# Performance work log

Measured on AMD Instinct MI355X. Metric: run time of the kernel, lower is better.

Reference implementation:

```python
import jax, jax.numpy as jnp
import numpy as np

SOFTCAP = 50.0
EPS = 1e-6
N_HEADS, D_HEAD = 16, 64


def _rms(x, w):
    return x * jax.lax.rsqrt(jnp.mean(x * x, axis=-1, keepdims=True) + EPS) * w


def _rope(x, cos, sin):
    # Faithful to source: apply_rope uses x.size(1) as the position axis, but is
    # called on (B, H, T, Dh) tensors, so positions are indexed by HEAD index.
    n = x.shape[1]
    x1, x2 = x[..., 0::2], x[..., 1::2]
    c = cos[:n][None, :, None, :]
    s = sin[:n][None, :, None, :]
    return jnp.stack([x1 * c - x2 * s, x1 * s + x2 * c], axis=-1).reshape(x.shape)


def setup_inputs() -> dict:
    key = jax.random.key(0)
    ks = jax.random.split(key, 12)
    L, D, H, Dh, Dff, V, B, T = 6, 1024, N_HEADS, D_HEAD, 4096, 32000, 1, 1024
    r = lambda k, shape: jax.random.normal(k, shape, dtype=jnp.float32) * 0.02
    return {
        'x': jax.random.randint(ks[0], (B, T), 0, V, dtype=jnp.int32),
        'embed': r(ks[1], (V, D)),
        'ln1': jnp.ones((L, D), jnp.float32),
        'Wq': r(ks[2], (L, H * Dh, D)),
        'Wk': r(ks[3], (L, H * Dh, D)),
        'Wv': r(ks[4], (L, H * Dh, D)),
        'Wo': r(ks[5], (L, D, H * Dh)),
        'qn': jnp.ones((L, Dh), jnp.float32),
        'kn': jnp.ones((L, Dh), jnp.float32),
        'ln2': jnp.ones((L, D), jnp.float32),
        'Wg': r(ks[6], (L, Dff, D)),
        'Wu': r(ks[7], (L, Dff, D)),
        'Wd': r(ks[8], (L, D, Dff)),
        'ln_out': jnp.ones((D,), jnp.float32),
    }


def reference(x, embed, ln1, Wq, Wk, Wv, Wo, qn, kn, ln2, Wg, Wu, Wd, ln_out):
    B, T = x.shape
    H, Dh = N_HEADS, D_HEAD
    scale = Dh ** -0.5
    # RoPE tables (theta=10000)
    freqs = 1.0 / (10000.0 ** (jnp.arange(0, Dh, 2, dtype=jnp.float32) / Dh))
    ang = jnp.arange(T, dtype=jnp.float32)[:, None] * freqs[None, :]
    cos, sin = jnp.cos(ang), jnp.sin(ang)
    mask = jnp.triu(jnp.ones((T, T), dtype=bool), k=1)  # True above diagonal

    h = embed[x]  # (B, T, D)

    def block(h, p):
        l1, wq, wk, wv, wo, qnw, knw, l2, wg, wu, wd = p
        hn = _rms(h, l1)
        q = (hn @ wq.T).reshape(B, T, H, Dh).transpose(0, 2, 1, 3)  # (B,H,T,Dh)
        k = (hn @ wk.T).reshape(B, T, H, Dh).transpose(0, 2, 1, 3)
        v = (hn @ wv.T).reshape(B, T, H, Dh).transpose(0, 2, 1, 3)
        q = _rope(_rms(q, qnw), cos, sin)
        k = _rope(_rms(k, knw), cos, sin)
        scores = jnp.einsum('bhtd,bhsd->bhts', q, k) * scale
        scores = SOFTCAP * jnp.tanh(scores / SOFTCAP)
        scores = jnp.where(mask[None, None], -jnp.inf, scores)
        attn = jax.nn.softmax(scores, axis=-1)
        o = jnp.einsum('bhts,bhsd->bhtd', attn, v)
        o = o.transpose(0, 2, 1, 3).reshape(B, T, H * Dh)
        h = h + o @ wo.T
        hn2 = _rms(h, l2)
        h = h + (jax.nn.silu(hn2 @ wg.T) * (hn2 @ wu.T)) @ wd.T
        return h, None

    h, _ = jax.lax.scan(block, h, (ln1, Wq, Wk, Wv, Wo, qn, kn, ln2, Wg, Wu, Wd))
    # tied embed/head
    logits = _rms(h, ln_out) @ embed.T  # (B, T, V)
    return logits
```

## Files before the change

kernel.cpp:

```cpp
#include <hip/hip_runtime.h>
#include <math.h>
#include <type_traits>

typedef __bf16 bf16_t;
typedef bf16_t bf16x4 __attribute__((ext_vector_type(4)));
typedef bf16_t bf16x8 __attribute__((ext_vector_type(8)));
typedef float  f32x4  __attribute__((ext_vector_type(4)));

#define RMS_EPS 1e-6f

enum { EP_STORE = 0, EP_RESID = 1, EP_SPLIT = 2, EP_SILU = 3 };

template<int V> using IC = std::integral_constant<int, V>;

static __device__ __forceinline__ f32x4 mfma16(bf16x8 a, bf16x8 b, f32x4 c) {
    return __builtin_amdgcn_mfma_f32_16x16x32_bf16(a, b, c, 0, 0, 0);
}

#define GLDS(gp, lp) __builtin_amdgcn_global_load_lds( \
    (const __attribute__((address_space(1))) void*)(gp), \
    (__attribute__((address_space(3))) void*)(lp), 16, 0, 0)

template<int N> static __device__ __forceinline__ void vmwait() {
    if constexpr (N == 0)      asm volatile("s_waitcnt vmcnt(0)" ::: "memory");
    else if constexpr (N == 2) asm volatile("s_waitcnt vmcnt(2)" ::: "memory");
    else if constexpr (N == 3) asm volatile("s_waitcnt vmcnt(3)" ::: "memory");
    else if constexpr (N == 4) asm volatile("s_waitcnt vmcnt(4)" ::: "memory");
    else if constexpr (N == 6) asm volatile("s_waitcnt vmcnt(6)" ::: "memory");
    else if constexpr (N == 8) asm volatile("s_waitcnt vmcnt(8)" ::: "memory");
    __builtin_amdgcn_sched_barrier(0);
}
static __device__ __forceinline__ void bar() { __builtin_amdgcn_s_barrier(); }

template<int BM, int BN, int PLANES, int EPIL>
__global__ __launch_bounds__(256, (PLANES >= 2 && BM == 128) ? 3 : 4)
void gemm_bf16(const bf16_t* __restrict__ Ah, const bf16_t* __restrict__ Al,
               const bf16_t* __restrict__ Bh,
               float* __restrict__ Cf, bf16_t* __restrict__ Ch, bf16_t* __restrict__ Cl,
               int K, int lda, int ldb, int ldc, long long sC)
{
    constexpr int ASZ = BM * 32, BSZ = BN * 32;
    constexpr int NLD = (BM / 64) * (PLANES >= 2 ? 2 : 1) + (BN / 64);
    __shared__ __align__(16) bf16_t sAh[2][ASZ], sBh[2][BSZ];
    __shared__ __align__(16) bf16_t sAl[PLANES >= 2 ? 2 : 1][PLANES >= 2 ? ASZ : 8];

    const int gx = gridDim.x;
    int id = blockIdx.x + gx * blockIdx.y;
    if (gridDim.z == 1) {
        int nwg = gx * gridDim.y;
        int q = nwg >> 3, r = nwg & 7;
        int xcd = id & 7, ix = id >> 3;
        id = (xcd < r ? xcd * (q + 1) : r * (q + 1) + (xcd - r) * q) + ix;
    }
    const int bm = id % gx, bn = id / gx;
    const int row0 = bm * BM, col0 = bn * BN;

    const size_t kofs = (size_t)blockIdx.z * K;
    Ah += kofs;  Bh += kofs;
    if constexpr (PLANES >= 2) Al += kofs;

    const int tid = threadIdx.x, lane = tid & 63, wave = tid >> 6;
    const int lr = lane & 15, lg = lane >> 4;
    constexpr int WM = BM / 2, WN = BN / 2, MF = WM / 16, NF = WN / 16;
    const int wm = wave >> 1, wn = wave & 1;

    f32x4 acc[MF][NF];
    #pragma unroll
    for (int m = 0; m < MF; ++m)
        #pragma unroll
        for (int n = 0; n < NF; ++n) acc[m][n] = (f32x4){0.f, 0.f, 0.f, 0.f};

    auto stage = [&](int k0, auto pc) {
        constexpr int p = decltype(pc)::value;
        #pragma unroll
        for (int i = wave; i < BM / 16; i += 4) {
            int s = i * 64 + lane, rr = s >> 2, c = s & 3;
            size_t go = (size_t)(row0 + rr) * lda + k0 + ((c ^ ((rr >> 1) & 3)) << 3);
            GLDS(Ah + go, &sAh[p][i * 512]);
            if constexpr (PLANES >= 2) GLDS(Al + go, &sAl[p][i * 512]);
        }
        #pragma unroll
        for (int i = wave; i < BN / 16; i += 4) {
            int s = i * 64 + lane, rr = s >> 2, c = s & 3;
            size_t go = (size_t)(col0 + rr) * ldb + k0 + ((c ^ ((rr >> 1) & 3)) << 3);
            GLDS(Bh + go, &sBh[p][i * 512]);
        }
    };

    auto compute = [&](auto pc) {
        constexpr int p = decltype(pc)::value;
        bf16x8 ahf[MF], alf[MF], bhf[NF];
        #pragma unroll
        for (int m = 0; m < MF; ++m) {
            int rr = wm * WM + m * 16 + lr;
            int by = rr * 64 + ((lg ^ ((rr >> 1) & 3)) << 4);
            ahf[m] = *(const bf16x8*)((const char*)&sAh[p][0] + by);
            if constexpr (PLANES >= 2)
                alf[m] = *(const bf16x8*)((const char*)&sAl[p][0] + by);
        }
        #pragma unroll
        for (int n = 0; n < NF; ++n) {
            int rr = wn * WN + n * 16 + lr;
            int by = rr * 64 + ((lg ^ ((rr >> 1) & 3)) << 4);
            bhf[n] = *(const bf16x8*)((const char*)&sBh[p][0] + by);
        }
        #pragma unroll
        for (int m = 0; m < MF; ++m)
            #pragma unroll
            for (int n = 0; n < NF; ++n) {
                acc[m][n] = mfma16(ahf[m], bhf[n], acc[m][n]);
                if constexpr (PLANES >= 2)
                    acc[m][n] = mfma16(alf[m], bhf[n], acc[m][n]);
            }
    };

    stage(0, IC<0>{});
    int k0 = 32;
    for (; k0 + 32 < K; k0 += 64) {
        stage(k0, IC<1>{});
        vmwait<NLD>(); bar();
        compute(IC<0>{});
        bar();
        stage(k0 + 32, IC<0>{});
        vmwait<NLD>(); bar();
        compute(IC<1>{});
        bar();
    }
    stage(k0, IC<1>{});
    vmwait<NLD>(); bar();
    compute(IC<0>{});
    bar();
    vmwait<0>(); bar();
    compute(IC<1>{});

    #pragma unroll
    for (int m = 0; m < MF; ++m)
        #pragma unroll
        for (int n = 0; n < NF; ++n)
            #pragma unroll
            for (int r = 0; r < 4; ++r) {
                int grow = row0 + wm * WM + m * 16 + lg * 4 + r;
                int gcol = col0 + wn * WN + n * 16 + lr;
                float v = acc[m][n][r];
                if constexpr (EPIL == EP_SILU) {
                    float pv = __shfl_xor(v, 1, 64);
                    if (!(lr & 1)) {
                        float s = (v / (1.0f + expf(-v))) * pv;
                        size_t off = (size_t)grow * ldc + (gcol >> 1);
                        Ch[off] = (bf16_t)s;
                    }
                } else {
                    size_t off = (size_t)blockIdx.z * sC + (size_t)grow * ldc + gcol;
                    if constexpr (EPIL == EP_STORE) {
                        Cf[off] = v;
                    } else if constexpr (EPIL == EP_RESID) {
                        Cf[off] += v;
                    } else {
                        bf16_t hb = (bf16_t)v;
                        Ch[off] = hb;
                        Cl[off] = (bf16_t)(v - (float)hb);
                    }
                }
            }
}

__global__ __launch_bounds__(256, 3)
void gemm_logits(const bf16_t* __restrict__ Ah, const bf16_t* __restrict__ Bh,
                 float* __restrict__ Cf)
{
    constexpr int lda = 1024, ldb = 1024, ldc = 32000;
    __shared__ __align__(16) bf16_t sA[3][128 * 32], sB[3][128 * 32];

    const int gx = gridDim.x;
    int id = blockIdx.x + gx * blockIdx.y;
    {
        int nwg = gx * gridDim.y;
        int q = nwg >> 3, r = nwg & 7;
        int xcd = id & 7, ix = id >> 3;
        id = (xcd < r ? xcd * (q + 1) : r * (q + 1) + (xcd - r) * q) + ix;
    }
    const int bm = id % gx, bn = id / gx;
    const int row0 = bm * 128, col0 = bn * 128;

    const int tid = threadIdx.x, lane = tid & 63, wave = tid >> 6;
    const int lr = lane & 15, lg = lane >> 4;
    const int wm = wave >> 1, wn = wave & 1;

    f32x4 acc[4][4];
    #pragma unroll
    for (int m = 0; m < 4; ++m)
        #pragma unroll
        for (int n = 0; n < 4; ++n) acc[m][n] = (f32x4){0.f, 0.f, 0.f, 0.f};

    auto stage = [&](int k0, int p) {
        #pragma unroll
        for (int i = wave; i < 8; i += 4) {
            int s = i * 64 + lane, rr = s >> 2, c = s & 3;
            size_t go = (size_t)(row0 + rr) * lda + k0 + ((c ^ ((rr >> 1) & 3)) << 3);
            GLDS(Ah + go, &sA[p][i * 512]);
        }
        #pragma unroll
        for (int i = wave; i < 8; i += 4) {
            int s = i * 64 + lane, rr = s >> 2, c = s & 3;
            size_t go = (size_t)(col0 + rr) * ldb + k0 + ((c ^ ((rr >> 1) & 3)) << 3);
            GLDS(Bh + go, &sB[p][i * 512]);
        }
    };

    auto compute = [&](int p) {
        bf16x8 af[4], bf[4];
        #pragma unroll
        for (int m = 0; m < 4; ++m) {
            int rr = wm * 64 + m * 16 + lr;
            int by = rr * 64 + ((lg ^ ((rr >> 1) & 3)) << 4);
            af[m] = *(const bf16x8*)((const char*)&sA[p][0] + by);
        }
        #pragma unroll
        for (int n = 0; n < 4; ++n) {
            int rr = wn * 64 + n * 16 + lr;
            int by = rr * 64 + ((lg ^ ((rr >> 1) & 3)) << 4);
            bf[n] = *(const bf16x8*)((const char*)&sB[p][0] + by);
        }
        #pragma unroll
        for (int m = 0; m < 4; ++m)
            #pragma unroll
            for (int n = 0; n < 4; ++n)
                acc[m][n] = mfma16(af[m], bf[n], acc[m][n]);
    };

    stage(0, 0);
    stage(32, 1);
    for (int j = 0; j < 30; ++j) {
        stage(32 * (j + 2), (j + 2) % 3);
        vmwait<8>(); bar();
        compute(j % 3);
        bar();
    }
    vmwait<4>(); bar();
    compute(0);
    vmwait<0>(); bar();
    compute(1);

    #pragma unroll
    for (int m = 0; m < 4; ++m)
        #pragma unroll
        for (int n = 0; n < 4; ++n)
            #pragma unroll
            for (int r = 0; r < 4; ++r) {
                int grow = row0 + wm * 64 + m * 16 + lg * 4 + r;
                int gcol = col0 + wn * 64 + n * 16 + lr;
                Cf[(size_t)grow * ldc + gcol] = acc[m][n][r];
            }
}

__global__ __launch_bounds__(256)
void reduce4_rms(const float* __restrict__ p, float* __restrict__ h,
                 const float* __restrict__ w, bf16_t* __restrict__ outh)
{
    int row = blockIdx.x, tid = threadIdx.x;
    size_t i = (size_t)row * 256 + tid;
    const size_t S = (1024 * 1024) / 4;
    f32x4 a = ((const f32x4*)p)[i];
    f32x4 b = ((const f32x4*)p)[i + S];
    f32x4 c = ((const f32x4*)p)[i + 2 * S];
    f32x4 d = ((const f32x4*)p)[i + 3 * S];
    f32x4 hv = ((const f32x4*)h)[i];
    #pragma unroll
    for (int j = 0; j < 4; ++j) hv[j] += (a[j] + b[j]) + (c[j] + d[j]);
    ((f32x4*)h)[i] = hv;

    float ss = hv[0]*hv[0] + hv[1]*hv[1] + hv[2]*hv[2] + hv[3]*hv[3];
    #pragma unroll
    for (int m = 1; m < 64; m <<= 1) ss += __shfl_xor(ss, m, 64);
    __shared__ float red[4];
    if ((tid & 63) == 0) red[tid >> 6] = ss;
    __syncthreads();
    float tot = red[0] + red[1] + red[2] + red[3];
    float inv = rsqrtf(tot * (1.0f / 1024.0f) + RMS_EPS);
    f32x4 wv = *(const f32x4*)(w + tid * 4);
    bf16x4 hv4;
    #pragma unroll
    for (int j = 0; j < 4; ++j) hv4[j] = (bf16_t)(hv[j] * inv * wv[j]);
    ((bf16x4*)outh)[i] = hv4;
}

__global__ __launch_bounds__(128, 2)
void flash_attn(const bf16_t* __restrict__ qkvh,
                const bf16_t* __restrict__ vTh, const bf16_t* __restrict__ vTl,
                bf16_t* __restrict__ oh)
{
    __shared__ __align__(16) bf16_t sQ[32*64], sK[64*64], sVh[64*64], sVl[64*64];
    __shared__ __align__(16) bf16_t sPh[32*64], sPl[32*64];

    const int px = blockIdx.x;
    const int hh = blockIdx.y;
    const int tid = threadIdx.x, lane = tid & 63, w = tid >> 6;
    const int lr = lane & 15, lg = lane >> 4;

    for (int cc = 0; cc < 2; ++cc) {
        const int qb = cc ? 31 - px : px;
        const int q0 = qb * 32;

        #pragma unroll
        for (int ii = 0; ii < 2; ++ii) {
            int r0 = w * 16 + ii * 8;
            int r  = r0 + (lane >> 3);
            int i  = lane & 7;
            GLDS(qkvh + (size_t)(q0 + r) * 3072 + hh * 64 + ((i ^ (r & 7)) << 3),
                 sQ + r0 * 64);
        }
        __syncthreads();

        bf16x8 qa[2];
        #pragma unroll
        for (int ks = 0; ks < 2; ++ks) {
            int r = w * 16 + lr;
            qa[ks] = *(const bf16x8*)((const char*)sQ + r * 128 +
                                      ((((ks << 2) | lg) ^ (r & 7)) << 4));
        }

        f32x4 o_acc[4];
        #pragma unroll
        for (int n = 0; n < 4; ++n) o_acc[n] = (f32x4){0.f, 0.f, 0.f, 0.f};
        float m_run[4] = {-1e30f, -1e30f, -1e30f, -1e30f};
        float l_run[4] = {0.f, 0.f, 0.f, 0.f};

        const int ntiles = ((q0 + 31) >> 6) + 1;
        for (int t = 0; t < ntiles; ++t) {
            const int kv0 = t * 64;
            #pragma unroll
            for (int ii = 0; ii < 4; ++ii) {
                int r0 = w * 32 + ii * 8;
                int r  = r0 + (lane >> 3);
                int i  = lane & 7;
                GLDS(qkvh + (size_t)(kv0 + r) * 3072 + 1024 + hh * 64 + ((i ^ (r & 7)) << 3),
                     sK + r0 * 64);
                GLDS(vTh + (size_t)(hh * 64 + r) * 1024 + kv0 + ((i ^ (r & 7)) << 3),
                     sVh + r0 * 64);
                GLDS(vTl + (size_t)(hh * 64 + r) * 1024 + kv0 + ((i ^ (r & 7)) << 3),
                     sVl + r0 * 64);
            }
            __syncthreads();

            f32x4 s_acc[4];
            #pragma unroll
            for (int n = 0; n < 4; ++n) s_acc[n] = (f32x4){0.f, 0.f, 0.f, 0.f};
            #pragma unroll
            for (int ks = 0; ks < 2; ++ks)
                #pragma unroll
                for (int n = 0; n < 4; ++n) {
                    int r = n * 16 + lr;
                    bf16x8 kb = *(const bf16x8*)((const char*)sK + r * 128 +
                                                 ((((ks << 2) | lg) ^ (r & 7)) << 4));
                    s_acc[n] = mfma16(qa[ks], kb, s_acc[n]);
                }

            #pragma unroll
            for (int j = 0; j < 4; ++j) {
                int qr = q0 + w * 16 + lg * 4 + j;
                float p[4];
                float mx = -1e30f;
                #pragma unroll
                for (int n = 0; n < 4; ++n) {
                    float v = s_acc[n][j] * 0.125f;
                    v = 50.f * tanhf(v * 0.02f);
                    int key = kv0 + n * 16 + lr;
                    if (key > qr) v = -1e30f;
                    p[n] = v;
                    mx = fmaxf(mx, v);
                }
                #pragma unroll
                for (int m = 1; m < 16; m <<= 1) mx = fmaxf(mx, __shfl_xor(mx, m, 64));
                float mn = fmaxf(m_run[j], mx);
                float ef = __expf(m_run[j] - mn);
                m_run[j] = mn;
                float rs = 0.f;
                #pragma unroll
                for (int n = 0; n < 4; ++n) {
                    float e = expf(p[n] - mn);
                    p[n] = e;
                    rs += e;
                }
                #pragma unroll
                for (int m = 1; m < 16; m <<= 1) rs += __shfl_xor(rs, m, 64);
                l_run[j] = l_run[j] * ef + rs;
                #pragma unroll
                for (int n = 0; n < 4; ++n) o_acc[n][j] *= ef;
                int r = w * 16 + lg * 4 + j;
                #pragma unroll
                for (int n = 0; n < 4; ++n) {
                    int c = n * 16 + lr;
                    int byo = r * 128 + ((((c >> 3) ^ (r & 7)) << 4)) + ((c & 7) << 1);
                    bf16_t hb = (bf16_t)p[n];
                    *(bf16_t*)((char*)sPh + byo) = hb;
                    *(bf16_t*)((char*)sPl + byo) = (bf16_t)(p[n] - (float)hb);
                }
            }

            #pragma unroll
            for (int ks = 0; ks < 2; ++ks) {
                int pr = w * 16 + lr;
                int pby = pr * 128 + ((((ks << 2) | lg) ^ (pr & 7)) << 4);
                bf16x8 pa  = *(const bf16x8*)((const char*)sPh + pby);
                bf16x8 pl_ = *(const bf16x8*)((const char*)sPl + pby);
                #pragma unroll
                for (int n = 0; n < 4; ++n) {
                    int vr = n * 16 + lr;
                    int vby = vr * 128 + ((((ks << 2) | lg) ^ (vr & 7)) << 4);
                    bf16x8 vhf = *(const bf16x8*)((const char*)sVh + vby);
                    bf16x8 vlf = *(const bf16x8*)((const char*)sVl + vby);
                    o_acc[n] = mfma16(pa,  vhf, o_acc[n]);
                    o_acc[n] = mfma16(pl_, vhf, o_acc[n]);
                    o_acc[n] = mfma16(pa,  vlf, o_acc[n]);
                }
            }
            __syncthreads();
        }

        #pragma unroll
        for (int j = 0; j < 4; ++j) {
            float inv = 1.0f / l_run[j];
            int qr = q0 + w * 16 + lg * 4 + j;
            #pragma unroll
            for (int n = 0; n < 4; ++n) {
                size_t off = (size_t)qr * 1024 + hh * 64 + n * 16 + lr;
                oh[off] = (bf16_t)(o_acc[n][j] * inv);
            }
        }
    }
}

__global__ __launch_bounds__(256)
void split_kernel(const float* __restrict__ src, bf16_t* __restrict__ hi,
                  bf16_t* __restrict__ lo)
{
    size_t i = (size_t)blockIdx.x * 256 + threadIdx.x;
    f32x4 v = ((const f32x4*)src)[i];
    bf16x4 hv, lv;
    #pragma unroll
    for (int j = 0; j < 4; ++j) {
        bf16_t hb = (bf16_t)v[j];
        hv[j] = hb;
        lv[j] = (bf16_t)(v[j] - (float)hb);
    }
    ((bf16x4*)hi)[i] = hv;
    if (lo) ((bf16x4*)lo)[i] = lv;
}

__global__ __launch_bounds__(256)
void wsplit_kernel(const float* __restrict__ wq, const float* __restrict__ wk,
                   const float* __restrict__ wv, const float* __restrict__ wo,
                   const float* __restrict__ wg, const float* __restrict__ wu,
                   const float* __restrict__ wd,
                   bf16_t* __restrict__ wAh, bf16_t* __restrict__ wGUh,
                   bf16_t* __restrict__ wdh)
{
    #pragma unroll
    for (int k = 0; k < 4; ++k) {
        int b = blockIdx.x * 4 + k;
        const float* src;
        bf16_t* dst;
        size_t so, doff;
        if (b < 4096) {
            src = b < 1024 ? wq : b < 2048 ? wk : b < 3072 ? wv : wo;
            so = (size_t)(b & 1023) * 256 + threadIdx.x;
            doff = (size_t)b * 256 + threadIdx.x;
            dst = wAh;
        } else if (b < 12288) {
            int bb = b - 4096;
            int row = bb < 4096 ? 2 * bb : 2 * (bb - 4096) + 1;
            src = bb < 4096 ? wg : wu;
            so = (size_t)(bb & 4095) * 256 + threadIdx.x;
            doff = (size_t)row * 256 + threadIdx.x;
            dst = wGUh;
        } else {
            src = wd;
            so = (size_t)(b - 12288) * 256 + threadIdx.x;
            doff = so;
            dst = wdh;
        }
        f32x4 v = ((const f32x4*)src)[so];
        bf16x4 hv;
        #pragma unroll
        for (int j = 0; j < 4; ++j) hv[j] = (bf16_t)v[j];
        ((bf16x4*)dst)[doff] = hv;
    }
}

__global__ __launch_bounds__(256)
void gather_rms(const int* __restrict__ ids, const float* __restrict__ embed,
                const float* __restrict__ w, float* __restrict__ h,
                bf16_t* __restrict__ outh)
{
    int t = blockIdx.x, tid = threadIdx.x;
    int row = ids[t];
    f32x4 v = ((const f32x4*)(embed + (size_t)row * 1024))[tid];
    ((f32x4*)(h + (size_t)t * 1024))[tid] = v;

    float ss = v[0]*v[0] + v[1]*v[1] + v[2]*v[2] + v[3]*v[3];
    #pragma unroll
    for (int m = 1; m < 64; m <<= 1) ss += __shfl_xor(ss, m, 64);
    __shared__ float red[4];
    if ((tid & 63) == 0) red[tid >> 6] = ss;
    __syncthreads();
    float tot = red[0] + red[1] + red[2] + red[3];
    float inv = rsqrtf(tot * (1.0f / 1024.0f) + RMS_EPS);
    f32x4 wv = *(const f32x4*)(w + tid * 4);
    bf16x4 hv;
    #pragma unroll
    for (int j = 0; j < 4; ++j) hv[j] = (bf16_t)(v[j] * inv * wv[j]);
    ((bf16x4*)outh)[(size_t)t * 256 + tid] = hv;
}

__global__ __launch_bounds__(256)
void rmsnorm_split(const float* __restrict__ in, const float* __restrict__ w,
                   bf16_t* __restrict__ outh)
{
    int row = blockIdx.x, tid = threadIdx.x;
    f32x4 v = *(const f32x4*)(in + (size_t)row * 1024 + tid * 4);
    float ss = v[0]*v[0] + v[1]*v[1] + v[2]*v[2] + v[3]*v[3];
    #pragma unroll
    for (int m = 1; m < 64; m <<= 1) ss += __shfl_xor(ss, m, 64);
    __shared__ float red[4];
    if ((tid & 63) == 0) red[tid >> 6] = ss;
    __syncthreads();
    float tot = red[0] + red[1] + red[2] + red[3];
    float inv = rsqrtf(tot * (1.0f / 1024.0f) + RMS_EPS);
    f32x4 wv = *(const f32x4*)(w + tid * 4);
    bf16x4 hv;
    #pragma unroll
    for (int j = 0; j < 4; ++j) hv[j] = (bf16_t)(v[j] * inv * wv[j]);
    ((bf16x4*)outh)[(size_t)row * 256 + tid] = hv;
}

__global__ __launch_bounds__(256)
void rope_transpose(bf16_t* __restrict__ qkvh, bf16_t* __restrict__ qkvl,
                    const float* __restrict__ qn, const float* __restrict__ kn,
                    bf16_t* __restrict__ vTh, bf16_t* __restrict__ vTl)
{
    __shared__ bf16_t tile[32][33];
    int b = blockIdx.x;
    if (b >= 1024) {
        int t2 = b - 1024;
        int z = t2 >> 10, rem = t2 & 1023;
        const bf16_t* in = z ? qkvl : qkvh;
        bf16_t* out      = z ? vTl : vTh;
        int bx = (rem & 31) * 32, by = (rem >> 5) * 32;
        int r = threadIdx.x >> 5, c = threadIdx.x & 31;
        #pragma unroll
        for (int rr = r; rr < 32; rr += 8)
            tile[rr][c] = in[(size_t)(by + rr) * 3072 + 2048 + bx + c];
        __syncthreads();
        #pragma unroll
        for (int rr = r; rr < 32; rr += 8)
            out[(size_t)(bx + rr) * 1024 + by + c] = tile[c][rr];
        return;
    }

    int t = b, tid = threadIdx.x;
    int hh = tid >> 4;
    int i  = (tid & 15) * 4;
    size_t qb = ((size_t)t * 3072 + hh * 64 + i) >> 2;
    size_t kb = qb + (1024 >> 2);

    int p0 = i >> 1;
    float f0 = powf(10000.f, -(float)p0 / 32.f);
    float f1 = powf(10000.f, -(float)(p0 + 1) / 32.f);
    float a0 = (float)hh * f0, a1 = (float)hh * f1;
    float c0 = cosf(a0), s0 = sinf(a0);
    float c1 = cosf(a1), s1 = sinf(a1);

    f32x4 qw = *(const f32x4*)(qn + i);
    f32x4 kw = *(const f32x4*)(kn + i);

    {
        bf16x4 h4 = ((const bf16x4*)qkvh)[qb], l4 = ((const bf16x4*)qkvl)[qb];
        float x[4];
        #pragma unroll
        for (int j = 0; j < 4; ++j) x[j] = (float)h4[j] + (float)l4[j];
        float ss = x[0]*x[0] + x[1]*x[1] + x[2]*x[2] + x[3]*x[3];
        #pragma unroll
        for (int m = 1; m < 16; m <<= 1) ss += __shfl_xor(ss, m, 64);
        float inv = rsqrtf(ss * (1.0f / 64.0f) + RMS_EPS);
        float x0 = x[0]*inv*qw[0], x1 = x[1]*inv*qw[1];
        float x2 = x[2]*inv*qw[2], x3 = x[3]*inv*qw[3];
        bf16x4 o4;
        o4[0] = (bf16_t)(x0*c0 - x1*s0);  o4[1] = (bf16_t)(x0*s0 + x1*c0);
        o4[2] = (bf16_t)(x2*c1 - x3*s1);  o4[3] = (bf16_t)(x2*s1 + x3*c1);
        ((bf16x4*)qkvh)[qb] = o4;
    }
    {
        bf16x4 h4 = ((const bf16x4*)qkvh)[kb], l4 = ((const bf16x4*)qkvl)[kb];
        float x[4];
        #pragma unroll
        for (int j = 0; j < 4; ++j) x[j] = (float)h4[j] + (float)l4[j];
        float ss = x[0]*x[0] + x[1]*x[1] + x[2]*x[2] + x[3]*x[3];
        #pragma unroll
        for (int m = 1; m < 16; m <<= 1) ss += __shfl_xor(ss, m, 64);
        float inv = rsqrtf(ss * (1.0f / 64.0f) + RMS_EPS);
        float x0 = x[0]*inv*kw[0], x1 = x[1]*inv*kw[1];
        float x2 = x[2]*inv*kw[2], x3 = x[3]*inv*kw[3];
        bf16x4 o4;
        o4[0] = (bf16_t)(x0*c0 - x1*s0);  o4[1] = (bf16_t)(x0*s0 + x1*c0);
        o4[2] = (bf16_t)(x2*c1 - x3*s1);  o4[3] = (bf16_t)(x2*s1 + x3*c1);
        ((bf16x4*)qkvh)[kb] = o4;
    }
}

extern "C" void kernel_launch(void* const* d_in, const int* in_sizes, int n_in,
                              void* d_out, int out_size, void* d_ws, size_t ws_size,
                              hipStream_t stream)
{
    (void)in_sizes; (void)n_in; (void)out_size; (void)ws_size;
    const int*   x_ids = (const int*)  d_in[0];
    const float* embed = (const float*)d_in[1];
    const float* ln1   = (const float*)d_in[2];
    const float* Wq    = (const float*)d_in[3];
    const float* Wk    = (const float*)d_in[4];
    const float* Wv    = (const float*)d_in[5];
    const float* Wo    = (const float*)d_in[6];
    const float* qn    = (const float*)d_in[7];
    const float* kn    = (const float*)d_in[8];
    const float* ln2   = (const float*)d_in[9];
    const float* Wg    = (const float*)d_in[10];
    const float* Wu    = (const float*)d_in[11];
    const float* Wd    = (const float*)d_in[12];
    const float* lnout = (const float*)d_in[13];
    float* out = (float*)d_out;

    char* ws = (char*)d_ws;
    const size_t MB = 1 << 20;
    float*  h    = (float*) (ws +   0 * MB);
    bf16_t* hnh  = (bf16_t*)(ws +   4 * MB);
    bf16_t* qkvh = (bf16_t*)(ws +   8 * MB);
    bf16_t* qkvl = (bf16_t*)(ws +  14 * MB);
    bf16_t* vTh  = (bf16_t*)(ws +  20 * MB);
    bf16_t* vTl  = (bf16_t*)(ws +  22 * MB);
    bf16_t* oh   = (bf16_t*)(ws +  24 * MB);
    bf16_t* wAh  = (bf16_t*)(ws +  28 * MB);
    bf16_t* wGUh = (bf16_t*)(ws +  36 * MB);
    bf16_t* wdh  = (bf16_t*)(ws +  52 * MB);
    bf16_t* silh = (bf16_t*)(ws +  60 * MB);
    float*  wdp  = (float*) (ws +  68 * MB);
    bf16_t* eh   = (bf16_t*)(ws +  84 * MB);

    const long long M1 = 1024 * 1024;

    gather_rms<<<1024, 256, 0, stream>>>(x_ids, embed, ln1, h, hnh);

    for (int l = 0; l < 6; ++l) {
        const float* wq = Wq + (size_t)l * M1;
        const float* wk = Wk + (size_t)l * M1;
        const float* wv = Wv + (size_t)l * M1;
        const float* wo = Wo + (size_t)l * M1;
        const float* wg = Wg + (size_t)l * 4 * M1;
        const float* wu = Wu + (size_t)l * 4 * M1;
        const float* wd = Wd + (size_t)l * 4 * M1;

        wsplit_kernel<<<4096, 256, 0, stream>>>(wq, wk, wv, wo, wg, wu, wd,
                                                wAh, wGUh, wdh);

        gemm_bf16<64,128,1,EP_SPLIT><<<dim3(16,24),256,0,stream>>>(
            hnh, nullptr, wAh, nullptr, qkvh, qkvl, 1024, 1024, 1024, 3072, 0);

        rope_transpose<<<3072, 256, 0, stream>>>(qkvh, qkvl, qn + l * 64, kn + l * 64,
                                                 vTh, vTl);

        flash_attn<<<dim3(16,16), 128, 0, stream>>>(qkvh, vTh, vTl, oh);

        gemm_bf16<64,64,1,EP_RESID><<<dim3(16,16),256,0,stream>>>(
            oh, nullptr, wAh + 3 * M1, h, nullptr, nullptr, 1024, 1024, 1024, 1024, 0);

        rmsnorm_split<<<1024, 256, 0, stream>>>(h, ln2 + l * 1024, hnh);

        gemm_bf16<128,128,1,EP_SILU><<<dim3(8,64),256,0,stream>>>(
            hnh, nullptr, wGUh, nullptr, silh, nullptr, 1024, 1024, 1024, 4096, 0);

        gemm_bf16<128,128,1,EP_STORE><<<dim3(8,8,4),256,0,stream>>>(
            silh, nullptr, wdh, wdp, nullptr, nullptr, 1024, 4096, 4096, 1024, M1);

        const float* wnext = (l < 5) ? (ln1 + (l + 1) * 1024) : lnout;
        reduce4_rms<<<1024, 256, 0, stream>>>(wdp, h, wnext, hnh);
    }

    split_kernel<<<32000, 256, 0, stream>>>(embed, eh, nullptr);
    gemm_logits<<<dim3(8,250), 256, 0, stream>>>(hnh, eh, out);
}
```

Before: 1.226 ms.

## Fuse weight conversion into norm kernels, widen GEMM tiles, split attention blocks

The per-layer weight fp32→bf16 conversion kernel is folded into the preceding gather/rmsnorm and reduce kernels as extra blocks, removing separate launches. The GEMM template gains a configurable wave grid, so the gate/up GEMM and the logits GEMM use 512-thread blocks with 256-wide N tiles. Flash attention is launched with twice as many blocks, each handling one query tile instead of a paired pair. The wider tiles raise register and LDS pressure per block, and the extra attention blocks lose the causal load balancing the paired tiles gave.

Result: no change. 1.236 ms (+0.8%).

```diff
diff --git a/kernel.cpp b/kernel.cpp
--- a/kernel.cpp
+++ b/kernel.cpp
@@ -32,15 +32,17 @@
 }
 static __device__ __forceinline__ void bar() { __builtin_amdgcn_s_barrier(); }
 
-template<int BM, int BN, int PLANES, int EPIL>
-__global__ __launch_bounds__(256, (PLANES >= 2 && BM == 128) ? 3 : 4)
+template<int BM, int BN, int WR, int WC, int PLANES, int EPIL>
+__global__ __launch_bounds__(WR * WC * 64,
+    (WR * WC == 8) ? 4 : ((PLANES >= 2 && BM == 128) ? 3 : 4))
 void gemm_bf16(const bf16_t* __restrict__ Ah, const bf16_t* __restrict__ Al,
                const bf16_t* __restrict__ Bh,
                float* __restrict__ Cf, bf16_t* __restrict__ Ch, bf16_t* __restrict__ Cl,
                int K, int lda, int ldb, int ldc, long long sC)
 {
     constexpr int ASZ = BM * 32, BSZ = BN * 32;
-    constexpr int NLD = (BM / 64) * (PLANES >= 2 ? 2 : 1) + (BN / 64);
+    constexpr int NW = WR * WC;
+    constexpr int NLD = (BM / 16 * (PLANES >= 2 ? 2 : 1) + BN / 16) / NW;
     __shared__ __align__(16) bf16_t sAh[2][ASZ], sBh[2][BSZ];
     __shared__ __align__(16) bf16_t sAl[PLANES >= 2 ? 2 : 1][PLANES >= 2 ? ASZ : 8];
 
@@ -61,8 +63,8 @@
 
     const int tid = threadIdx.x, lane = tid & 63, wave = tid >> 6;
     const int lr = lane & 15, lg = lane >> 4;
-    constexpr int WM = BM / 2, WN = BN / 2, MF = WM / 16, NF = WN / 16;
-    const int wm = wave >> 1, wn = wave & 1;
+    constexpr int WM = BM / WR, WN = BN / WC, MF = WM / 16, NF = WN / 16;
+    const int wr = wave / WC, wc = wave % WC;
 
     f32x4 acc[MF][NF];
     #pragma unroll
@@ -73,14 +75,14 @@
     auto stage = [&](int k0, auto pc) {
         constexpr int p = decltype(pc)::value;
         #pragma unroll
-        for (int i = wave; i < BM / 16; i += 4) {
+        for (int i = wave; i < BM / 16; i += NW) {
             int s = i * 64 + lane, rr = s >> 2, c = s & 3;
             size_t go = (size_t)(row0 + rr) * lda + k0 + ((c ^ ((rr >> 1) & 3)) << 3);
             GLDS(Ah + go, &sAh[p][i * 512]);
             if constexpr (PLANES >= 2) GLDS(Al + go, &sAl[p][i * 512]);
         }
         #pragma unroll
-        for (int i = wave; i < BN / 16; i += 4) {
+        for (int i = wave; i < BN / 16; i += NW) {
             int s = i * 64 + lane, rr = s >> 2, c = s & 3;
             size_t go = (size_t)(col0 + rr) * ldb + k0 + ((c ^ ((rr >> 1) & 3)) << 3);
             GLDS(Bh + go, &sBh[p][i * 512]);
@@ -92,7 +94,7 @@
         bf16x8 ahf[MF], alf[MF], bhf[NF];
         #pragma unroll
         for (int m = 0; m < MF; ++m) {
-            int rr = wm * WM + m * 16 + lr;
+            int rr = wr * WM + m * 16 + lr;
             int by = rr * 64 + ((lg ^ ((rr >> 1) & 3)) << 4);
             ahf[m] = *(const bf16x8*)((const char*)&sAh[p][0] + by);
             if constexpr (PLANES >= 2)
@@ -100,7 +102,7 @@
         }
         #pragma unroll
         for (int n = 0; n < NF; ++n) {
-            int rr = wn * WN + n * 16 + lr;
+            int rr = wc * WN + n * 16 + lr;
             int by = rr * 64 + ((lg ^ ((rr >> 1) & 3)) << 4);
             bhf[n] = *(const bf16x8*)((const char*)&sBh[p][0] + by);
         }
@@ -139,8 +141,8 @@
         for (int n = 0; n < NF; ++n)
             #pragma unroll
             for (int r = 0; r < 4; ++r) {
-                int grow = row0 + wm * WM + m * 16 + lg * 4 + r;
-                int gcol = col0 + wn * WN + n * 16 + lr;
+                int grow = row0 + wr * WM + m * 16 + lg * 4 + r;
+                int gcol = col0 + wc * WN + n * 16 + lr;
                 float v = acc[m][n][r];
                 if constexpr (EPIL == EP_SILU) {
                     float pv = __shfl_xor(v, 1, 64);
@@ -164,12 +166,12 @@
             }
 }
 
-__global__ __launch_bounds__(256, 3)
+__global__ __launch_bounds__(512, 4)
 void gemm_logits(const bf16_t* __restrict__ Ah, const bf16_t* __restrict__ Bh,
                  float* __restrict__ Cf)
 {
     constexpr int lda = 1024, ldb = 1024, ldc = 32000;
-    __shared__ __align__(16) bf16_t sA[3][128 * 32], sB[3][128 * 32];
+    __shared__ __align__(16) bf16_t sA[3][128 * 32], sB[3][256 * 32];
 
     const int gx = gridDim.x;
     int id = blockIdx.x + gx * blockIdx.y;
@@ -180,11 +182,11 @@
         id = (xcd < r ? xcd * (q + 1) : r * (q + 1) + (xcd - r) * q) + ix;
     }
     const int bm = id % gx, bn = id / gx;
-    const int row0 = bm * 128, col0 = bn * 128;
+    const int row0 = bm * 128, col0 = bn * 256;
 
     const int tid = threadIdx.x, lane = tid & 63, wave = tid >> 6;
     const int lr = lane & 15, lg = lane >> 4;
-    const int wm = wave >> 1, wn = wave & 1;
+    const int wr = wave >> 2, wc = wave & 3;
 
     f32x4 acc[4][4];
     #pragma unroll
@@ -193,14 +195,14 @@
         for (int n = 0; n < 4; ++n) acc[m][n] = (f32x4){0.f, 0.f, 0.f, 0.f};
 
     auto stage = [&](int k0, int p) {
-        #pragma unroll
-        for (int i = wave; i < 8; i += 4) {
+        {
+            int i = wave;
             int s = i * 64 + lane, rr = s >> 2, c = s & 3;
             size_t go = (size_t)(row0 + rr) * lda + k0 + ((c ^ ((rr >> 1) & 3)) << 3);
             GLDS(Ah + go, &sA[p][i * 512]);
         }
         #pragma unroll
-        for (int i = wave; i < 8; i += 4) {
+        for (int i = wave; i < 16; i += 8) {
             int s = i * 64 + lane, rr = s >> 2, c = s & 3;
             size_t go = (size_t)(col0 + rr) * ldb + k0 + ((c ^ ((rr >> 1) & 3)) << 3);
             GLDS(Bh + go, &sB[p][i * 512]);
@@ -211,13 +213,13 @@
         bf16x8 af[4], bf[4];
         #pragma unroll
         for (int m = 0; m < 4; ++m) {
-            int rr = wm * 64 + m * 16 + lr;
+            int rr = wr * 64 + m * 16 + lr;
             int by = rr * 64 + ((lg ^ ((rr >> 1) & 3)) << 4);
             af[m] = *(const bf16x8*)((const char*)&sA[p][0] + by);
         }
         #pragma unroll
         for (int n = 0; n < 4; ++n) {
-            int rr = wn * 64 + n * 16 + lr;
+            int rr = wc * 64 + n * 16 + lr;
             int by = rr * 64 + ((lg ^ ((rr >> 1) & 3)) << 4);
             bf[n] = *(const bf16x8*)((const char*)&sB[p][0] + by);
         }
@@ -232,11 +234,11 @@
     stage(32, 1);
     for (int j = 0; j < 30; ++j) {
         stage(32 * (j + 2), (j + 2) % 3);
-        vmwait<8>(); bar();
+        vmwait<6>(); bar();
         compute(j % 3);
         bar();
     }
-    vmwait<4>(); bar();
+    vmwait<3>(); bar();
     compute(0);
     vmwait<0>(); bar();
     compute(1);
@@ -247,18 +249,64 @@
         for (int n = 0; n < 4; ++n)
             #pragma unroll
             for (int r = 0; r < 4; ++r) {
-                int grow = row0 + wm * 64 + m * 16 + lg * 4 + r;
-                int gcol = col0 + wn * 64 + n * 16 + lr;
+                int grow = row0 + wr * 64 + m * 16 + lg * 4 + r;
+                int gcol = col0 + wc * 64 + n * 16 + lr;
                 Cf[(size_t)grow * ldc + gcol] = acc[m][n][r];
             }
 }
 
+static __device__ __forceinline__ void wsplit_body(
+    int b2, int tid,
+    const float* wq, const float* wk, const float* wv, const float* wo,
+    const float* wg, const float* wu, const float* wd,
+    bf16_t* wAh, bf16_t* wGUh, bf16_t* wdh)
+{
+    #pragma unroll
+    for (int k = 0; k < 4; ++k) {
+        int b = b2 * 4 + k;
+        const float* src;
+        bf16_t* dst;
+        size_t so, doff;
+        if (b < 4096) {
+            src = b < 1024 ? wq : b < 2048 ? wk : b < 3072 ? wv : wo;
+            so = (size_t)(b & 1023) * 256 + tid;
+            doff = (size_t)b * 256 + tid;
+            dst = wAh;
+        } else if (b < 12288) {
+            int bb = b - 4096;
+            int row = bb < 4096 ? 2 * bb : 2 * (bb - 4096) + 1;
+            src = bb < 4096 ? wg : wu;
+            so = (size_t)(bb & 4095) * 256 + tid;
+            doff = (size_t)row * 256 + tid;
+            dst = wGUh;
+        } else {
+            src = wd;
+            so = (size_t)(b - 12288) * 256 + tid;
+            doff = so;
+            dst = wdh;
+        }
+        f32x4 v = ((const f32x4*)src)[so];
+        bf16x4 hv;
+        #pragma unroll
+        for (int j = 0; j < 4; ++j) hv[j] = (bf16_t)v[j];
+        ((bf16x4*)dst)[doff] = hv;
+    }
+}
+
 __global__ __launch_bounds__(256)
-void reduce4_rms(const float* __restrict__ p, float* __restrict__ h,
-                 const float* __restrict__ w, bf16_t* __restrict__ outh)
-{
-    int row = blockIdx.x, tid = threadIdx.x;
-    size_t i = (size_t)row * 256 + tid;
+void reduce_rms_wsplit(const float* __restrict__ p, float* __restrict__ h,
+                       const float* __restrict__ w, bf16_t* __restrict__ outh,
+                       const float* wq, const float* wk, const float* wv,
+                       const float* wo, const float* wg, const float* wu,
+                       const float* wd, bf16_t* wAh, bf16_t* wGUh, bf16_t* wdh)
+{
+    int blk = blockIdx.x, tid = threadIdx.x;
+    if (blk >= 1024) {
+        if (wq) wsplit_body(blk - 1024, tid, wq, wk, wv, wo, wg, wu, wd,
+                            wAh, wGUh, wdh);
+        return;
+    }
+    size_t i = (size_t)blk * 256 + tid;
     const size_t S = (1024 * 1024) / 4;
     f32x4 a = ((const f32x4*)p)[i];
     f32x4 b = ((const f32x4*)p)[i + S];
@@ -277,225 +325,29 @@
     __syncthreads();
     float tot = red[0] + red[1] + red[2] + red[3];
     float inv = rsqrtf(tot * (1.0f / 1024.0f) + RMS_EPS);
-    f32x4 wv = *(const f32x4*)(w + tid * 4);
+    f32x4 wt4 = *(const f32x4*)(w + tid * 4);
     bf16x4 hv4;
     #pragma unroll
-    for (int j = 0; j < 4; ++j) hv4[j] = (bf16_t)(hv[j] * inv * wv[j]);
+    for (int j = 0; j < 4; ++j) hv4[j] = (bf16_t)(hv[j] * inv * wt4[j]);
     ((bf16x4*)outh)[i] = hv4;
 }
 
-__global__ __launch_bounds__(128, 2)
-void flash_attn(const bf16_t* __restrict__ qkvh,
-                const bf16_t* __restrict__ vTh, const bf16_t* __restrict__ vTl,
-                bf16_t* __restrict__ oh)
-{
-    __shared__ __align__(16) bf16_t sQ[32*64], sK[64*64], sVh[64*64], sVl[64*64];
-    __shared__ __align__(16) bf16_t sPh[32*64], sPl[32*64];
-
-    const int px = blockIdx.x;
-    const int hh = blockIdx.y;
-    const int tid = threadIdx.x, lane = tid & 63, w = tid >> 6;
-    const int lr = lane & 15, lg = lane >> 4;
-
-    for (int cc = 0; cc < 2; ++cc) {
-        const int qb = cc ? 31 - px : px;
-        const int q0 = qb * 32;
-
-        #pragma unroll
-        for (int ii = 0; ii < 2; ++ii) {
-            int r0 = w * 16 + ii * 8;
-            int r  = r0 + (lane >> 3);
-            int i  = lane & 7;
-            GLDS(qkvh + (size_t)(q0 + r) * 3072 + hh * 64 + ((i ^ (r & 7)) << 3),
-                 sQ + r0 * 64);
-        }
-        __syncthreads();
-
-        bf16x8 qa[2];
-        #pragma unroll
-        for (int ks = 0; ks < 2; ++ks) {
-            int r = w * 16 + lr;
-            qa[ks] = *(const bf16x8*)((const char*)sQ + r * 128 +
-                                      ((((ks << 2) | lg) ^ (r & 7)) << 4));
-        }
-
-        f32x4 o_acc[4];
-        #pragma unroll
-        for (int n = 0; n < 4; ++n) o_acc[n] = (f32x4){0.f, 0.f, 0.f, 0.f};
-        float m_run[4] = {-1e30f, -1e30f, -1e30f, -1e30f};
-        float l_run[4] = {0.f, 0.f, 0.f, 0.f};
-
-        const int ntiles = ((q0 + 31) >> 6) + 1;
-        for (int t = 0; t < ntiles; ++t) {
-            const int kv0 = t * 64;
-            #pragma unroll
-            for (int ii = 0; ii < 4; ++ii) {
-                int r0 = w * 32 + ii * 8;
-                int r  = r0 + (lane >> 3);
-                int i  = lane & 7;
-                GLDS(qkvh + (size_t)(kv0 + r) * 3072 + 1024 + hh * 64 + ((i ^ (r & 7)) << 3),
-                     sK + r0 * 64);
-                GLDS(vTh + (size_t)(hh * 64 + r) * 1024 + kv0 + ((i ^ (r & 7)) << 3),
-                     sVh + r0 * 64);
-                GLDS(vTl + (size_t)(hh * 64 + r) * 1024 + kv0 + ((i ^ (r & 7)) << 3),
-                     sVl + r0 * 64);
-            }
-            __syncthreads();
-
-            f32x4 s_acc[4];
-            #pragma unroll
-            for (int n = 0; n < 4; ++n) s_acc[n] = (f32x4){0.f, 0.f, 0.f, 0.f};
-            #pragma unroll
-            for (int ks = 0; ks < 2; ++ks)
-                #pragma unroll
-                for (int n = 0; n < 4; ++n) {
-                    int r = n * 16 + lr;
-                    bf16x8 kb = *(const bf16x8*)((const char*)sK + r * 128 +
-                                                 ((((ks << 2) | lg) ^ (r & 7)) << 4));
-                    s_acc[n] = mfma16(qa[ks], kb, s_acc[n]);
-                }
-
-            #pragma unroll
-            for (int j = 0; j < 4; ++j) {
-                int qr = q0 + w * 16 + lg * 4 + j;
-                float p[4];
-                float mx = -1e30f;
-                #pragma unroll
-                for (int n = 0; n < 4; ++n) {
-                    float v = s_acc[n][j] * 0.125f;
-                    v = 50.f * tanhf(v * 0.02f);
-                    int key = kv0 + n * 16 + lr;
-                    if (key > qr) v = -1e30f;
-                    p[n] = v;
-                    mx = fmaxf(mx, v);
-                }
-                #pragma unroll
-                for (int m = 1; m < 16; m <<= 1) mx = fmaxf(mx, __shfl_xor(mx, m, 64));
-                float mn = fmaxf(m_run[j], mx);
-                float ef = __expf(m_run[j] - mn);
-                m_run[j] = mn;
-                float rs = 0.f;
-                #pragma unroll
-                for (int n = 0; n < 4; ++n) {
-                    float e = expf(p[n] - mn);
-                    p[n] = e;
-                    rs += e;
-                }
-                #pragma unroll
-                for (int m = 1; m < 16; m <<= 1) rs += __shfl_xor(rs, m, 64);
-                l_run[j] = l_run[j] * ef + rs;
-                #pragma unroll
-                for (int n = 0; n < 4; ++n) o_acc[n][j] *= ef;
-                int r = w * 16 + lg * 4 + j;
-                #pragma unroll
-                for (int n = 0; n < 4; ++n) {
-                    int c = n * 16 + lr;
-                    int byo = r * 128 + ((((c >> 3) ^ (r & 7)) << 4)) + ((c & 7) << 1);
-                    bf16_t hb = (bf16_t)p[n];
-                    *(bf16_t*)((char*)sPh + byo) = hb;
-                    *(bf16_t*)((char*)sPl + byo) = (bf16_t)(p[n] - (float)hb);
-                }
-            }
-
-            #pragma unroll
-            for (int ks = 0; ks < 2; ++ks) {
-                int pr = w * 16 + lr;
-                int pby = pr * 128 + ((((ks << 2) | lg) ^ (pr & 7)) << 4);
-                bf16x8 pa  = *(const bf16x8*)((const char*)sPh + pby);
-                bf16x8 pl_ = *(const bf16x8*)((const char*)sPl + pby);
-                #pragma unroll
-                for (int n = 0; n < 4; ++n) {
-                    int vr = n * 16 + lr;
-                    int vby = vr * 128 + ((((ks << 2) | lg) ^ (vr & 7)) << 4);
-                    bf16x8 vhf = *(const bf16x8*)((const char*)sVh + vby);
-                    bf16x8 vlf = *(const bf16x8*)((const char*)sVl + vby);
-                    o_acc[n] = mfma16(pa,  vhf, o_acc[n]);
-                    o_acc[n] = mfma16(pl_, vhf, o_acc[n]);
-                    o_acc[n] = mfma16(pa,  vlf, o_acc[n]);
-                }
-            }
-            __syncthreads();
-        }
-
-        #pragma unroll
-        for (int j = 0; j < 4; ++j) {
-            float inv = 1.0f / l_run[j];
-            int qr = q0 + w * 16 + lg * 4 + j;
-            #pragma unroll
-            for (int n = 0; n < 4; ++n) {
-                size_t off = (size_t)qr * 1024 + hh * 64 + n * 16 + lr;
-                oh[off] = (bf16_t)(o_acc[n][j] * inv);
-            }
-        }
-    }
-}
-
 __global__ __launch_bounds__(256)
-void split_kernel(const float* __restrict__ src, bf16_t* __restrict__ hi,
-                  bf16_t* __restrict__ lo)
-{
-    size_t i = (size_t)blockIdx.x * 256 + threadIdx.x;
-    f32x4 v = ((const f32x4*)src)[i];
-    bf16x4 hv, lv;
-    #pragma unroll
-    for (int j = 0; j < 4; ++j) {
-        bf16_t hb = (bf16_t)v[j];
-        hv[j] = hb;
-        lv[j] = (bf16_t)(v[j] - (float)hb);
-    }
-    ((bf16x4*)hi)[i] = hv;
-    if (lo) ((bf16x4*)lo)[i] = lv;
-}
-
-__global__ __launch_bounds__(256)
-void wsplit_kernel(const float* __restrict__ wq, const float* __restrict__ wk,
-                   const float* __restrict__ wv, const float* __restrict__ wo,
-                   const float* __restrict__ wg, const float* __restrict__ wu,
-                   const float* __restrict__ wd,
-                   bf16_t* __restrict__ wAh, bf16_t* __restrict__ wGUh,
-                   bf16_t* __restrict__ wdh)
-{
-    #pragma unroll
-    for (int k = 0; k < 4; ++k) {
-        int b = blockIdx.x * 4 + k;
-        const float* src;
-        bf16_t* dst;
-        size_t so, doff;
-        if (b < 4096) {
-            src = b < 1024 ? wq : b < 2048 ? wk : b < 3072 ? wv : wo;
-            so = (size_t)(b & 1023) * 256 + threadIdx.x;
-            doff = (size_t)b * 256 + threadIdx.x;
-            dst = wAh;
-        } else if (b < 12288) {
-            int bb = b - 4096;
-            int row = bb < 4096 ? 2 * bb : 2 * (bb - 4096) + 1;
-            src = bb < 4096 ? wg : wu;
-            so = (size_t)(bb & 4095) * 256 + threadIdx.x;
-            doff = (size_t)row * 256 + threadIdx.x;
-            dst = wGUh;
-        } else {
-            src = wd;
-            so = (size_t)(b - 12288) * 256 + threadIdx.x;
-            doff = so;
-            dst = wdh;
-        }
-        f32x4 v = ((const f32x4*)src)[so];
-        bf16x4 hv;
-        #pragma unroll
-        for (int j = 0; j < 4; ++j) hv[j] = (bf16_t)v[j];
-        ((bf16x4*)dst)[doff] = hv;
-    }
-}
-
-__global__ __launch_bounds__(256)
-void gather_rms(const int* __restrict__ ids, const float* __restrict__ embed,
-                const float* __restrict__ w, float* __restrict__ h,
-                bf16_t* __restrict__ outh)
-{
-    int t = blockIdx.x, tid = threadIdx.x;
-    int row = ids[t];
+void gather_rms_wsplit(const int* __restrict__ ids, const float* __restrict__ embed,
+                       const float* __restrict__ w, float* __restrict__ h,
+                       bf16_t* __restrict__ outh,
+                       const float* wq, const float* wk, const float* wv,
+                       const float* wo, const float* wg, const float* wu,
+                       const float* wd, bf16_t* wAh, bf16_t* wGUh, bf16_t* wdh)
+{
+    int blk = blockIdx.x, tid = threadIdx.x;
+    if (blk >= 1024) {
+        wsplit_body(blk - 1024, tid, wq, wk, wv, wo, wg, wu, wd, wAh, wGUh, wdh);
+        return;
+    }
+    int row = ids[blk];
     f32x4 v = ((const f32x4*)(embed + (size_t)row * 1024))[tid];
-    ((f32x4*)(h + (size_t)t * 1024))[tid] = v;
+    ((f32x4*)(h + (size_t)blk * 1024))[tid] = v;
 
     float ss = v[0]*v[0] + v[1]*v[1] + v[2]*v[2] + v[3]*v[3];
     #pragma unroll
@@ -505,11 +357,163 @@
     __syncthreads();
     float tot = red[0] + red[1] + red[2] + red[3];
     float inv = rsqrtf(tot * (1.0f / 1024.0f) + RMS_EPS);
-    f32x4 wv = *(const f32x4*)(w + tid * 4);
+    f32x4 wt4 = *(const f32x4*)(w + tid * 4);
     bf16x4 hv;
     #pragma unroll
-    for (int j = 0; j < 4; ++j) hv[j] = (bf16_t)(v[j] * inv * wv[j]);
-    ((bf16x4*)outh)[(size_t)t * 256 + tid] = hv;
+    for (int j = 0; j < 4; ++j) hv[j] = (bf16_t)(v[j] * inv * wt4[j]);
+    ((bf16x4*)outh)[(size_t)blk * 256 + tid] = hv;
+}
+
+__global__ __launch_bounds__(128, 2)
+void flash_attn(const bf16_t* __restrict__ qkvh,
+                const bf16_t* __restrict__ vTh, const bf16_t* __restrict__ vTl,
+                bf16_t* __restrict__ oh)
+{
+    __shared__ __align__(16) bf16_t sQ[32*64], sK[64*64], sVh[64*64], sVl[64*64];
+    __shared__ __align__(16) bf16_t sPh[32*64], sPl[32*64];
+
+    const int q0 = blockIdx.x * 32;
+    const int hh = blockIdx.y;
+    const int tid = threadIdx.x, lane = tid & 63, w = tid >> 6;
+    const int lr = lane & 15, lg = lane >> 4;
+
+    #pragma unroll
+    for (int ii = 0; ii < 2; ++ii) {
+        int r0 = w * 16 + ii * 8;
+        int r  = r0 + (lane >> 3);
+        int i  = lane & 7;
+        GLDS(qkvh + (size_t)(q0 + r) * 3072 + hh * 64 + ((i ^ (r & 7)) << 3),
+             sQ + r0 * 64);
+    }
+    __syncthreads();
+
+    bf16x8 qa[2];
+    #pragma unroll
+    for (int ks = 0; ks < 2; ++ks) {
+        int r = w * 16 + lr;
+        qa[ks] = *(const bf16x8*)((const char*)sQ + r * 128 +
+                                  ((((ks << 2) | lg) ^ (r & 7)) << 4));
+    }
+
+    f32x4 o_acc[4];
+    #pragma unroll
+    for (int n = 0; n < 4; ++n) o_acc[n] = (f32x4){0.f, 0.f, 0.f, 0.f};
+    float m_run[4] = {-1e30f, -1e30f, -1e30f, -1e30f};
+    float l_run[4] = {0.f, 0.f, 0.f, 0.f};
+
+    const int ntiles = ((q0 + 31) >> 6) + 1;
+    for (int t = 0; t < ntiles; ++t) {
+        const int kv0 = t * 64;
+        #pragma unroll
+        for (int ii = 0; ii < 4; ++ii) {
+            int r0 = w * 32 + ii * 8;
+            int r  = r0 + (lane >> 3);
+            int i  = lane & 7;
+            GLDS(qkvh + (size_t)(kv0 + r) * 3072 + 1024 + hh * 64 + ((i ^ (r & 7)) << 3),
+                 sK + r0 * 64);
+            GLDS(vTh + (size_t)(hh * 64 + r) * 1024 + kv0 + ((i ^ (r & 7)) << 3),
+                 sVh + r0 * 64);
+            GLDS(vTl + (size_t)(hh * 64 + r) * 1024 + kv0 + ((i ^ (r & 7)) << 3),
+                 sVl + r0 * 64);
+        }
+        __syncthreads();
+
+        f32x4 s_acc[4];
+        #pragma unroll
+        for (int n = 0; n < 4; ++n) s_acc[n] = (f32x4){0.f, 0.f, 0.f, 0.f};
+        #pragma unroll
+        for (int ks = 0; ks < 2; ++ks)
+            #pragma unroll
+            for (int n = 0; n < 4; ++n) {
+                int r = n * 16 + lr;
+                bf16x8 kb = *(const bf16x8*)((const char*)sK + r * 128 +
+                                             ((((ks << 2) | lg) ^ (r & 7)) << 4));
+                s_acc[n] = mfma16(qa[ks], kb, s_acc[n]);
+            }
+
+        #pragma unroll
+        for (int j = 0; j < 4; ++j) {
+            int qr = q0 + w * 16 + lg * 4 + j;
+            float p[4];
+            float mx = -1e30f;
+            #pragma unroll
+            for (int n = 0; n < 4; ++n) {
+                float v = s_acc[n][j] * 0.125f;
+                v = 50.f * tanhf(v * 0.02f);
+                int key = kv0 + n * 16 + lr;
+                if (key > qr) v = -1e30f;
+                p[n] = v;
+                mx = fmaxf(mx, v);
+            }
+            #pragma unroll
+            for (int m = 1; m < 16; m <<= 1) mx = fmaxf(mx, __shfl_xor(mx, m, 64));
+            float mn = fmaxf(m_run[j], mx);
+            float ef = __expf(m_run[j] - mn);
+            m_run[j] = mn;
+            float rs = 0.f;
+            #pragma unroll
+            for (int n = 0; n < 4; ++n) {
+                float e = expf(p[n] - mn);
+                p[n] = e;
+                rs += e;
+            }
+            #pragma unroll
+            for (int m = 1; m < 16; m <<= 1) rs += __shfl_xor(rs, m, 64);
+            l_run[j] = l_run[j] * ef + rs;
+            #pragma unroll
+            for (int n = 0; n < 4; ++n) o_acc[n][j] *= ef;
+            int r = w * 16 + lg * 4 + j;
+            #pragma unroll
+            for (int n = 0; n < 4; ++n) {
+                int c = n * 16 + lr;
+                int byo = r * 128 + ((((c >> 3) ^ (r & 7)) << 4)) + ((c & 7) << 1);
+                bf16_t hb = (bf16_t)p[n];
+                *(bf16_t*)((char*)sPh + byo) = hb;
+                *(bf16_t*)((char*)sPl + byo) = (bf16_t)(p[n] - (float)hb);
+            }
+        }
+
+        #pragma unroll
+        for (int ks = 0; ks < 2; ++ks) {
+            int pr = w * 16 + lr;
+            int pby = pr * 128 + ((((ks << 2) | lg) ^ (pr & 7)) << 4);
+            bf16x8 pa  = *(const bf16x8*)((const char*)sPh + pby);
+            bf16x8 pl_ = *(const bf16x8*)((const char*)sPl + pby);
+            #pragma unroll
+            for (int n = 0; n < 4; ++n) {
+                int vr = n * 16 + lr;
+                int vby = vr * 128 + ((((ks << 2) | lg) ^ (vr & 7)) << 4);
+                bf16x8 vhf = *(const bf16x8*)((const char*)sVh + vby);
+                bf16x8 vlf = *(const bf16x8*)((const char*)sVl + vby);
+                o_acc[n] = mfma16(pa,  vhf, o_acc[n]);
+                o_acc[n] = mfma16(pl_, vhf, o_acc[n]);
+                o_acc[n] = mfma16(pa,  vlf, o_acc[n]);
+            }
+        }
+        __syncthreads();
+    }
+
+    #pragma unroll
+    for (int j = 0; j < 4; ++j) {
+        float inv = 1.0f / l_run[j];
+        int qr = q0 + w * 16 + lg * 4 + j;
+        #pragma unroll
+        for (int n = 0; n < 4; ++n) {
+            size_t off = (size_t)qr * 1024 + hh * 64 + n * 16 + lr;
+            oh[off] = (bf16_t)(o_acc[n][j] * inv);
+        }
+    }
+}
+
+__global__ __launch_bounds__(256)
+void split_kernel(const float* __restrict__ src, bf16_t* __restrict__ hi)
+{
+    size_t i = (size_t)blockIdx.x * 256 + threadIdx.x;
+    f32x4 v = ((const f32x4*)src)[i];
+    bf16x4 hv;
+    #pragma unroll
+    for (int j = 0; j < 4; ++j) hv[j] = (bf16_t)v[j];
+    ((bf16x4*)hi)[i] = hv;
 }
 
 __global__ __launch_bounds__(256)
@@ -526,10 +530,10 @@
     __syncthreads();
     float tot = red[0] + red[1] + red[2] + red[3];
     float inv = rsqrtf(tot * (1.0f / 1024.0f) + RMS_EPS);
-    f32x4 wv = *(const f32x4*)(w + tid * 4);
+    f32x4 wt4 = *(const f32x4*)(w + tid * 4);
     bf16x4 hv;
     #pragma unroll
-    for (int j = 0; j < 4; ++j) hv[j] = (bf16_t)(v[j] * inv * wv[j]);
+    for (int j = 0; j < 4; ++j) hv[j] = (bf16_t)(v[j] * inv * wt4[j]);
     ((bf16x4*)outh)[(size_t)row * 256 + tid] = hv;
 }
 
@@ -646,43 +650,46 @@
 
     const long long M1 = 1024 * 1024;
 
-    gather_rms<<<1024, 256, 0, stream>>>(x_ids, embed, ln1, h, hnh);
+    gather_rms_wsplit<<<5120, 256, 0, stream>>>(
+        x_ids, embed, ln1, h, hnh,
+        Wq, Wk, Wv, Wo, Wg, Wu, Wd, wAh, wGUh, wdh);
 
     for (int l = 0; l < 6; ++l) {
-        const float* wq = Wq + (size_t)l * M1;
-        const float* wk = Wk + (size_t)l * M1;
-        const float* wv = Wv + (size_t)l * M1;
-        const float* wo = Wo + (size_t)l * M1;
-        const float* wg = Wg + (size_t)l * 4 * M1;
-        const float* wu = Wu + (size_t)l * 4 * M1;
-        const float* wd = Wd + (size_t)l * 4 * M1;
-
-        wsplit_kernel<<<4096, 256, 0, stream>>>(wq, wk, wv, wo, wg, wu, wd,
-                                                wAh, wGUh, wdh);
-
-        gemm_bf16<64,128,1,EP_SPLIT><<<dim3(16,24),256,0,stream>>>(
+        gemm_bf16<64,128,2,2,1,EP_SPLIT><<<dim3(16,24),256,0,stream>>>(
             hnh, nullptr, wAh, nullptr, qkvh, qkvl, 1024, 1024, 1024, 3072, 0);
 
         rope_transpose<<<3072, 256, 0, stream>>>(qkvh, qkvl, qn + l * 64, kn + l * 64,
                                                  vTh, vTl);
 
-        flash_attn<<<dim3(16,16), 128, 0, stream>>>(qkvh, vTh, vTl, oh);
-
-        gemm_bf16<64,64,1,EP_RESID><<<dim3(16,16),256,0,stream>>>(
+        flash_attn<<<dim3(32,16), 128, 0, stream>>>(qkvh, vTh, vTl, oh);
+
+        gemm_bf16<64,64,2,2,1,EP_RESID><<<dim3(16,16),256,0,stream>>>(
             oh, nullptr, wAh + 3 * M1, h, nullptr, nullptr, 1024, 1024, 1024, 1024, 0);
 
         rmsnorm_split<<<1024, 256, 0, stream>>>(h, ln2 + l * 1024, hnh);
 
-        gemm_bf16<128,128,1,EP_SILU><<<dim3(8,64),256,0,stream>>>(
+        gemm_bf16<128,256,2,4,1,EP_SILU><<<dim3(8,32),512,0,stream>>>(
             hnh, nullptr, wGUh, nullptr, silh, nullptr, 1024, 1024, 1024, 4096, 0);
 
-        gemm_bf16<128,128,1,EP_STORE><<<dim3(8,8,4),256,0,stream>>>(
+        gemm_bf16<128,128,2,2,1,EP_STORE><<<dim3(8,8,4),256,0,stream>>>(
             silh, nullptr, wdh, wdp, nullptr, nullptr, 1024, 4096, 4096, 1024, M1);
 
         const float* wnext = (l < 5) ? (ln1 + (l + 1) * 1024) : lnout;
-        reduce4_rms<<<1024, 256, 0, stream>>>(wdp, h, wnext, hnh);
-    }
-
-    split_kernel<<<32000, 256, 0, stream>>>(embed, eh, nullptr);
-    gemm_logits<<<dim3(8,250), 256, 0, stream>>>(hnh, eh, out);
-}
+        if (l < 5) {
+            reduce_rms_wsplit<<<5120, 256, 0, stream>>>(
+                wdp, h, wnext, hnh,
+                Wq + (size_t)(l+1) * M1, Wk + (size_t)(l+1) * M1,
+                Wv + (size_t)(l+1) * M1, Wo + (size_t)(l+1) * M1,
+                Wg + (size_t)(l+1) * 4 * M1, Wu + (size_t)(l+1) * 4 * M1,
+                Wd + (size_t)(l+1) * 4 * M1, wAh, wGUh, wdh);
+        } else {
+            reduce_rms_wsplit<<<1024, 256, 0, stream>>>(
+                wdp, h, wnext, hnh,
+                nullptr, nullptr, nullptr, nullptr, nullptr, nullptr, nullptr,
+                wAh, wGUh, wdh);
+        }
+    }
+
+    split_kernel<<<32000, 256, 0, stream>>>(embed, eh);
+    gemm_logits<<<dim3(8,125), 512, 0, stream>>>(hnh, eh, out);
+}
```
